# Kernel optimization log

Hardware: AMD Instinct MI355X
Metric: run time of the kernel (lower is better)

## Reference

```python
import jax, jax.numpy as jnp
import numpy as np

NEG_SLOPE = 0.2  # GAT LeakyReLU slope
EPS = 1e-16


def _pagat_conv(x, path_index, W, a, b, heads, out_ch, concat):
    """Path-augmented GAT conv: attention over (head, mid, tail) path triples,
    messages flow tail -> head, softmax-normalized per destination node."""
    N = x.shape[0]
    head, mid, tail = path_index[0], path_index[1], path_index[2]
    h = (x @ W).reshape(N, heads, out_ch)            # [N, H, C]
    # attention logits from all three path positions: [P, H]
    e = (jnp.einsum('phc,hc->ph', h[head], a[0])
         + jnp.einsum('phc,hc->ph', h[mid], a[1])
         + jnp.einsum('phc,hc->ph', h[tail], a[2]))
    e = jax.nn.leaky_relu(e, NEG_SLOPE)
    # segment softmax over paths grouped by destination (head) node
    m = jax.ops.segment_max(e, head, num_segments=N)  # [N, H]
    ex = jnp.exp(e - m[head])
    s = jax.ops.segment_sum(ex, head, num_segments=N)  # [N, H]
    alpha = ex / (s[head] + EPS)                       # [P, H]
    # aggregate tail features weighted by attention
    out = jax.ops.segment_sum(alpha[..., None] * h[tail], head, num_segments=N)  # [N, H, C]
    if concat:
        out = out.reshape(N, heads * out_ch)
    else:
        out = out.mean(axis=1)
    return out + b


def setup_inputs() -> dict:
    key = jax.random.key(0)
    ks = jax.random.split(key, 8)
    N, F_in, H, C, CLS, P = 100000, 500, 8, 16, 16, 1000000
    x = jax.random.normal(ks[0], (N, F_in), dtype=jnp.float32)
    path_index = jax.random.randint(ks[1], (3, P), 0, N, dtype=jnp.int32)
    W1 = jax.random.normal(ks[2], (F_in, H * C), dtype=jnp.float32) * 0.05
    a1 = jax.random.normal(ks[3], (3, H, C), dtype=jnp.float32) * 0.05
    b1 = jnp.zeros((H * C,), dtype=jnp.float32)
    W2 = jax.random.normal(ks[4], (H * C, CLS), dtype=jnp.float32) * 0.05
    a2 = jax.random.normal(ks[5], (3, 1, CLS), dtype=jnp.float32) * 0.05
    b2 = jnp.zeros((CLS,), dtype=jnp.float32)
    return {"x": x, "path_index": path_index, "W1": W1, "a1": a1, "b1": b1,
            "W2": W2, "a2": a2, "b2": b2}


def reference(x, path_index, W1, a1, b1, W2, a2, b2):
    # eval mode: dropout is identity
    h = _pagat_conv(x, path_index, W1, a1, b1, heads=8, out_ch=16, concat=True)
    h = jax.nn.elu(h)
    h = _pagat_conv(h, path_index, W2, a2, b2, heads=1, out_ch=16, concat=False)
    return jax.nn.log_softmax(h, axis=1)
```

## Files before the change

### kernel.cpp

```cpp
#include <hip/hip_runtime.h>
#include <hip/hip_bf16.h>

#define F_IN  500
#define HC    128
#define NHEAD 8
#define CDIM  16
#define NCLS  16
#define KPAD  512

static __device__ __forceinline__ float bf(const __hip_bfloat16 v) {
    return __bfloat162float(v);
}

static __device__ __forceinline__ unsigned int enc_f32(float f) {
    unsigned int u = __float_as_uint(f);
    return (u & 0x80000000u) ? ~u : (u | 0x80000000u);
}
static __device__ __forceinline__ float dec_f32(unsigned int u) {
    return __uint_as_float((u & 0x80000000u) ? (u & 0x7FFFFFFFu) : ~u);
}

typedef __bf16 bf16x8 __attribute__((ext_vector_type(8)));
typedef float f32x4 __attribute__((ext_vector_type(4)));

__global__ void zero_i32(int* __restrict__ p, int n) {
    int i = blockIdx.x * blockDim.x + threadIdx.x;
    if (i < n) p[i] = 0;
}

__global__ void transpose_w1(const float* __restrict__ W1,
                             __bf16* __restrict__ w1t_hi,
                             __bf16* __restrict__ w1t_lo)
{
    int id = blockIdx.x * 256 + threadIdx.x;
    int c = id >> 9, k = id & 511;
    float v = (k < F_IN) ? W1[k * HC + c] : 0.f;
    __bf16 h = (__bf16)v;
    w1t_hi[id] = h;
    w1t_lo[id] = (__bf16)(v - (float)h);
}

static __device__ __forceinline__ void split8(const float4 a, const float4 b,
                                              bf16x8& hi, bf16x8& lo) {
    float v[8] = {a.x, a.y, a.z, a.w, b.x, b.y, b.z, b.w};
#pragma unroll
    for (int j = 0; j < 8; j++) {
        __bf16 h = (__bf16)v[j];
        hi[j] = h;
        lo[j] = (__bf16)(v[j] - (float)h);
    }
}

__global__ __launch_bounds__(256) void gemm1_mfma(
    const float* __restrict__ x,
    const __bf16* __restrict__ w1t_hi, const __bf16* __restrict__ w1t_lo,
    __hip_bfloat16* __restrict__ h1, int N)
{
    const int wave = threadIdx.x >> 6, lane = threadIdx.x & 63;
    const int m = lane & 15, q = lane >> 4;
    const int row0 = blockIdx.x * 128 + wave * 32;

    long ra0 = row0 + m, ra1 = row0 + 16 + m;
    if (ra0 >= N) ra0 = 0;
    if (ra1 >= N) ra1 = 0;
    const float* pa0 = x + ra0 * F_IN + q * 8;
    const float* pa1 = x + ra1 * F_IN + q * 8;
    const __bf16* pbh = w1t_hi + (size_t)m * KPAD + q * 8;
    const __bf16* pbl = w1t_lo + (size_t)m * KPAD + q * 8;

    f32x4 acc[2][8];
#pragma unroll
    for (int i = 0; i < 2; i++)
#pragma unroll
        for (int t = 0; t < 8; t++) acc[i][t] = (f32x4){0.f, 0.f, 0.f, 0.f};

#pragma unroll
    for (int k0 = 0; k0 < 480; k0 += 32) {
        bf16x8 a0h, a0l, a1h, a1l;
        split8(*(const float4*)(pa0 + k0), *(const float4*)(pa0 + k0 + 4), a0h, a0l);
        split8(*(const float4*)(pa1 + k0), *(const float4*)(pa1 + k0 + 4), a1h, a1l);
#pragma unroll
        for (int t = 0; t < 8; t++) {
            bf16x8 bh = *(const bf16x8*)(pbh + t * 16 * KPAD + k0);
            bf16x8 bl = *(const bf16x8*)(pbl + t * 16 * KPAD + k0);
            acc[0][t] = __builtin_amdgcn_mfma_f32_16x16x32_bf16(a0h, bh, acc[0][t], 0, 0, 0);
            acc[0][t] = __builtin_amdgcn_mfma_f32_16x16x32_bf16(a0h, bl, acc[0][t], 0, 0, 0);
            acc[0][t] = __builtin_amdgcn_mfma_f32_16x16x32_bf16(a0l, bh, acc[0][t], 0, 0, 0);
            acc[1][t] = __builtin_amdgcn_mfma_f32_16x16x32_bf16(a1h, bh, acc[1][t], 0, 0, 0);
            acc[1][t] = __builtin_amdgcn_mfma_f32_16x16x32_bf16(a1h, bl, acc[1][t], 0, 0, 0);
            acc[1][t] = __builtin_amdgcn_mfma_f32_16x16x32_bf16(a1l, bh, acc[1][t], 0, 0, 0);
        }
    }
    {
        const float4 z4 = make_float4(0.f, 0.f, 0.f, 0.f);
        bf16x8 a0h, a0l, a1h, a1l;
        float4 u0 = (q < 3) ? *(const float4*)(pa0 + 480) : z4;
        float4 u1 = (q < 2) ? *(const float4*)(pa0 + 484) : z4;
        float4 w0 = (q < 3) ? *(const float4*)(pa1 + 480) : z4;
        float4 w1 = (q < 2) ? *(const float4*)(pa1 + 484) : z4;
        split8(u0, u1, a0h, a0l);
        split8(w0, w1, a1h, a1l);
#pragma unroll
        for (int t = 0; t < 8; t++) {
            bf16x8 bh = *(const bf16x8*)(pbh + t * 16 * KPAD + 480);
            bf16x8 bl = *(const bf16x8*)(pbl + t * 16 * KPAD + 480);
            acc[0][t] = __builtin_amdgcn_mfma_f32_16x16x32_bf16(a0h, bh, acc[0][t], 0, 0, 0);
            acc[0][t] = __builtin_amdgcn_mfma_f32_16x16x32_bf16(a0h, bl, acc[0][t], 0, 0, 0);
            acc[0][t] = __builtin_amdgcn_mfma_f32_16x16x32_bf16(a0l, bh, acc[0][t], 0, 0, 0);
            acc[1][t] = __builtin_amdgcn_mfma_f32_16x16x32_bf16(a1h, bh, acc[1][t], 0, 0, 0);
            acc[1][t] = __builtin_amdgcn_mfma_f32_16x16x32_bf16(a1h, bl, acc[1][t], 0, 0, 0);
            acc[1][t] = __builtin_amdgcn_mfma_f32_16x16x32_bf16(a1l, bh, acc[1][t], 0, 0, 0);
        }
    }
#pragma unroll
    for (int rt = 0; rt < 2; rt++) {
        int rbase = row0 + rt * 16 + q * 4;
#pragma unroll
        for (int t = 0; t < 8; t++) {
#pragma unroll
            for (int r = 0; r < 4; r++) {
                int row = rbase + r;
                if (row < N)
                    h1[(size_t)row * HC + t * 16 + m] = __float2bfloat16(acc[rt][t][r]);
            }
        }
    }
}

__global__ void dots1_kernel(const __hip_bfloat16* __restrict__ h1,
                             const float* __restrict__ a1,
                             float* __restrict__ d1, int N)
{
    int id = blockIdx.x * blockDim.x + threadIdx.x;
    if (id >= N * NHEAD) return;
    int n = id >> 3, h = id & 7;
    const __hip_bfloat16* hp = h1 + (size_t)n * HC + h * CDIM;
    float s0 = 0.f, s1 = 0.f, s2 = 0.f;
#pragma unroll
    for (int c = 0; c < CDIM; c++) {
        float v = bf(hp[c]);
        s0 += v * a1[(0 * NHEAD + h) * CDIM + c];
        s1 += v * a1[(1 * NHEAD + h) * CDIM + c];
        s2 += v * a1[(2 * NHEAD + h) * CDIM + c];
    }
    d1[id] = s0;
    d1[N * NHEAD + id] = s1;
    d1[2 * N * NHEAD + id] = s2;
}

__global__ void maxred_d1(const float* __restrict__ d1,
                          unsigned int* __restrict__ gmax, int N)
{
    __shared__ unsigned int sm[16];
    if (threadIdx.x < 16) sm[threadIdx.x] = 0;
    __syncthreads();
    int total = 2 * N * NHEAD;
    for (int i = blockIdx.x * blockDim.x + threadIdx.x; i < total;
         i += gridDim.x * blockDim.x) {
        float v = d1[(size_t)N * NHEAD + i];
        int slot = ((i >= N * NHEAD) ? 8 : 0) + (i & 7);
        atomicMax(&sm[slot], enc_f32(v));
    }
    __syncthreads();
    if (threadIdx.x < 16) atomicMax(&gmax[threadIdx.x], sm[threadIdx.x]);
}

__global__ void maxred_d2(const float* __restrict__ d2,
                          unsigned int* __restrict__ gmax2, int N)
{
    __shared__ unsigned int sm[2];
    if (threadIdx.x < 2) sm[threadIdx.x] = 0;
    __syncthreads();
    int total = 2 * N;
    for (int i = blockIdx.x * blockDim.x + threadIdx.x; i < total;
         i += gridDim.x * blockDim.x) {
        float v = d2[N + i];
        atomicMax(&sm[i >= N ? 1 : 0], enc_f32(v));
    }
    __syncthreads();
    if (threadIdx.x < 2) atomicMax(&gmax2[threadIdx.x], sm[threadIdx.x]);
}

__global__ void hist_kernel(const int* __restrict__ pidx, int* __restrict__ deg, int P) {
    int p = blockIdx.x * blockDim.x + threadIdx.x;
    if (p < P) atomicAdd(deg + pidx[p], 1);
}

__global__ void scan1_kernel(const int* __restrict__ deg, int* __restrict__ start,
                             int* __restrict__ bsum, int N) {
    __shared__ int sh[256];
    int i = blockIdx.x * 256 + threadIdx.x;
    int v = (i < N) ? deg[i] : 0;
    sh[threadIdx.x] = v;
    __syncthreads();
#pragma unroll
    for (int off = 1; off < 256; off <<= 1) {
        int x = (threadIdx.x >= off) ? sh[threadIdx.x - off] : 0;
        __syncthreads();
        sh[threadIdx.x] += x;
        __syncthreads();
    }
    if (i < N) start[i] = sh[threadIdx.x] - v;
    if (threadIdx.x == 255) bsum[blockIdx.x] = sh[255];
}

__global__ void scan2_kernel(int* __restrict__ bsum, int nb) {
    __shared__ int sh[512];
    int v = (threadIdx.x < nb) ? bsum[threadIdx.x] : 0;
    sh[threadIdx.x] = v;
    __syncthreads();
#pragma unroll
    for (int off = 1; off < 512; off <<= 1) {
        int x = (threadIdx.x >= off) ? sh[threadIdx.x - off] : 0;
        __syncthreads();
        sh[threadIdx.x] += x;
        __syncthreads();
    }
    if (threadIdx.x < nb) bsum[threadIdx.x] = sh[threadIdx.x] - v;
}

__global__ void scan3_kernel(int* __restrict__ start, const int* __restrict__ bsum, int N) {
    int i = blockIdx.x * 256 + threadIdx.x;
    if (i < N) start[i] += bsum[blockIdx.x];
}

__global__ void scatter_kernel(const int* __restrict__ pidx,
                               const int* __restrict__ start,
                               int* __restrict__ cursor,
                               int* __restrict__ csr, int P) {
    int p = blockIdx.x * blockDim.x + threadIdx.x;
    if (p >= P) return;
    int hd = pidx[p];
    int pos = atomicAdd(cursor + hd, 1);
    csr[start[hd] + pos] = p;
}

__global__ __launch_bounds__(256) void attn1_csr_kernel(
    const int* __restrict__ csr, const int* __restrict__ start,
    const int* __restrict__ deg, const int* __restrict__ pidx,
    const float* __restrict__ d1, const __hip_bfloat16* __restrict__ h1,
    const float* __restrict__ b1, const unsigned int* __restrict__ gmax,
    float* __restrict__ elu_out, int N, int P)
{
    int node = blockIdx.x * 4 + (threadIdx.x >> 6);
    if (node >= N) return;
    int lane = threadIdx.x & 63;
    int h = lane >> 3;
    int s0 = start[node], dg = deg[node];
    const float* d1m = d1 + (size_t)N * NHEAD;
    const float* d1t = d1 + (size_t)2 * N * NHEAD;
    const float dh = d1[node * NHEAD + h];
    float zub = dh + dec_f32(gmax[h]) + dec_f32(gmax[8 + h]);
    const float mxub = zub > 0.f ? zub : 0.2f * zub;

    float acc0 = 0.f, acc1 = 0.f, den = 0.f;
    for (int k0 = 0; k0 < dg; k0 += 8) {
        int kk = k0 + (lane & 7);
        bool valid = kk < dg;
        int p = csr[s0 + (valid ? kk : dg - 1)];
        int mid = pidx[P + p], tl = pidx[2 * P + p];
        float z = dh + d1m[mid * NHEAD + h] + d1t[tl * NHEAD + h];
        float e = z > 0.f ? z : 0.2f * z;
        float ex = valid ? __expf(e - mxub) : 0.f;
        den += ex;
        int kmax = dg - k0; if (kmax > 8) kmax = 8;
        for (int dk = 0; dk < kmax; dk++) {
            int tl_b = __shfl(tl, dk, 8);
            float ex_b = __shfl(ex, dk, 8);
            __hip_bfloat162 v = *(const __hip_bfloat162*)(h1 + (size_t)tl_b * HC + 2 * lane);
            acc0 += ex_b * bf(v.x);
            acc1 += ex_b * bf(v.y);
        }
    }
#pragma unroll
    for (int w = 1; w < 8; w <<= 1) den += __shfl_xor(den, w, 8);

    float inv = 1.f / (den + 1e-16f);
    int j0 = 2 * lane;
    float v0 = acc0 * inv + b1[j0];
    float v1 = acc1 * inv + b1[j0 + 1];
    v0 = v0 > 0.f ? v0 : __expf(v0) - 1.f;
    v1 = v1 > 0.f ? v1 : __expf(v1) - 1.f;
    *(float2*)(elu_out + (size_t)node * HC + j0) = make_float2(v0, v1);
}

__global__ __launch_bounds__(256) void layer2_kernel(
    const float* __restrict__ elu, const float* __restrict__ W2,
    const float* __restrict__ a2,
    float* __restrict__ h2, float* __restrict__ d2, int N)
{
    __shared__ float rows[16][HC + 1];
    __shared__ float h2s[16][NCLS + 1];
    const int n0 = blockIdx.x * 16;
    const int tid = threadIdx.x;
    for (int idx = tid; idx < 16 * HC; idx += 256) {
        int r = idx >> 7, c = idx & 127;
        rows[r][c] = (n0 + r < N) ? elu[(size_t)(n0 + r) * HC + c] : 0.f;
    }
    __syncthreads();
    int ln = tid >> 4, c = tid & 15;
    float acc = 0.f;
#pragma unroll 8
    for (int j = 0; j < HC; j++) acc += rows[ln][j] * W2[j * NCLS + c];
    h2s[ln][c] = acc;
    if (n0 + ln < N) h2[(size_t)(n0 + ln) * NCLS + c] = acc;
    __syncthreads();
    if (tid < 48) {
        int l = tid / 3, j = tid - l * 3;
        if (n0 + l < N) {
            float s = 0.f;
#pragma unroll
            for (int cc = 0; cc < NCLS; cc++) s += h2s[l][cc] * a2[j * NCLS + cc];
            d2[j * N + n0 + l] = s;
        }
    }
}

__global__ __launch_bounds__(256) void attn2_csr_kernel(
    const int* __restrict__ csr, const int* __restrict__ start,
    const int* __restrict__ deg, const int* __restrict__ pidx,
    const float* __restrict__ d2, const float* __restrict__ h2,
    const float* __restrict__ b2, const unsigned int* __restrict__ gmax2,
    float* __restrict__ out, int N, int P)
{
    int node = blockIdx.x * 16 + (threadIdx.x >> 4);
    if (node >= N) return;
    int c = threadIdx.x & 15;
    int s0 = start[node], dg = deg[node];
    const float dh = d2[node];
    const float* d2m = d2 + N;
    const float* d2t = d2 + 2 * N;
    float zub = dh + dec_f32(gmax2[0]) + dec_f32(gmax2[1]);
    const float mxub = zub > 0.f ? zub : 0.2f * zub;

    float acc = 0.f, den = 0.f;
    for (int k0 = 0; k0 < dg; k0 += 16) {
        int kk = k0 + c;
        bool valid = kk < dg;
        int p = csr[s0 + (valid ? kk : dg - 1)];
        int mid = pidx[P + p], tl = pidx[2 * P + p];
        float z = dh + d2m[mid] + d2t[tl];
        float e = z > 0.f ? z : 0.2f * z;
        float ex = valid ? __expf(e - mxub) : 0.f;
        den += ex;
        int kmax = dg - k0; if (kmax > 16) kmax = 16;
        for (int dk = 0; dk < kmax; dk++) {
            int tl_b = __shfl(tl, dk, 16);
            float ex_b = __shfl(ex, dk, 16);
            acc += ex_b * h2[(size_t)tl_b * NCLS + c];
        }
    }
#pragma unroll
    for (int w = 1; w < 16; w <<= 1) den += __shfl_xor(den, w, 16);

    float o = acc / (den + 1e-16f) + b2[c];
    float m2 = o;
#pragma unroll
    for (int w = 1; w < 16; w <<= 1) m2 = fmaxf(m2, __shfl_xor(m2, w, 16));
    float ex = __expf(o - m2), sm = ex;
#pragma unroll
    for (int w = 1; w < 16; w <<= 1) sm += __shfl_xor(sm, w, 16);
    float r = o - m2 - __logf(sm);
    out[(size_t)node * NCLS + c] = r;
}

extern "C" void kernel_launch(void* const* d_in, const int* in_sizes, int n_in,
                              void* d_out, int out_size, void* d_ws, size_t ws_size,
                              hipStream_t stream)
{
    const float* x  = (const float*)d_in[0];
    const int*   pi = (const int*)d_in[1];
    const float* W1 = (const float*)d_in[2];
    const float* a1 = (const float*)d_in[3];
    const float* b1 = (const float*)d_in[4];
    const float* W2 = (const float*)d_in[5];
    const float* a2 = (const float*)d_in[6];
    const float* b2 = (const float*)d_in[7];

    const int N = in_sizes[0] / F_IN;
    const int P = in_sizes[1] / 3;

    float* ws = (float*)d_ws;
    size_t off_h1     = 0;
    size_t off_d1     = (size_t)64 * N;
    size_t off_elu    = (size_t)88 * N;
    size_t off_h2     = (size_t)216 * N;
    size_t off_d2     = (size_t)232 * N;
    size_t off_deg    = (size_t)235 * N;
    size_t off_start  = (size_t)236 * N;
    size_t off_cursor = (size_t)237 * N;
    size_t off_gmax   = (size_t)238 * N;
    size_t off_bsum   = (size_t)238 * N + 32;
    size_t off_csr    = (size_t)238 * N + 32 + 1024;
    size_t off_w1th   = off_csr + P;
    size_t off_w1tl   = off_w1th + 32768;

    __hip_bfloat16* h1 = (__hip_bfloat16*)(ws + off_h1);
    float* d1   = ws + off_d1;
    float* elu  = ws + off_elu;
    float* h2   = ws + off_h2;
    float* d2   = ws + off_d2;
    int* deg    = (int*)(ws + off_deg);
    int* start  = (int*)(ws + off_start);
    int* cursor = (int*)(ws + off_cursor);
    unsigned int* gmax  = (unsigned int*)(ws + off_gmax);
    unsigned int* gmax2 = (unsigned int*)(ws + off_gmax) + 16;
    int* bsum   = (int*)(ws + off_bsum);
    int* csr    = (int*)(ws + off_csr);
    __bf16* w1t_hi = (__bf16*)(ws + off_w1th);
    __bf16* w1t_lo = (__bf16*)(ws + off_w1tl);

    const int BLK = 256;
    const int nb = (N + 255) / 256;

    transpose_w1<<<(HC * KPAD) / 256, 256, 0, stream>>>(W1, w1t_hi, w1t_lo);
    zero_i32<<<(3 * N + 32 + BLK - 1) / BLK, BLK, 0, stream>>>(deg, 3 * N + 32);
    gemm1_mfma<<<(N + 127) / 128, 256, 0, stream>>>(x, w1t_hi, w1t_lo, h1, N);
    dots1_kernel<<<(N * NHEAD + BLK - 1) / BLK, BLK, 0, stream>>>(h1, a1, d1, N);
    maxred_d1<<<1024, 256, 0, stream>>>(d1, gmax, N);
    hist_kernel<<<(P + BLK - 1) / BLK, BLK, 0, stream>>>(pi, deg, P);
    scan1_kernel<<<nb, 256, 0, stream>>>(deg, start, bsum, N);
    scan2_kernel<<<1, 512, 0, stream>>>(bsum, nb);
    scan3_kernel<<<nb, 256, 0, stream>>>(start, bsum, N);
    scatter_kernel<<<(P + BLK - 1) / BLK, BLK, 0, stream>>>(pi, start, cursor, csr, P);
    attn1_csr_kernel<<<(N + 3) / 4, 256, 0, stream>>>(csr, start, deg, pi, d1, h1, b1, gmax, elu, N, P);
    layer2_kernel<<<(N + 15) / 16, 256, 0, stream>>>(elu, W2, a2, h2, d2, N);
    maxred_d2<<<256, 256, 0, stream>>>(d2, gmax2, N);
    attn2_csr_kernel<<<(N + 15) / 16, 256, 0, stream>>>(csr, start, deg, pi, d2, h2, b2, gmax2,
                                                        (float*)d_out, N, P);
}
```

Baseline: 735.3 us.

## Stage GEMM1 tiles through LDS with double-buffered async global-to-LDS loads

New measurement: 701.3 us. -4.6%, faster.

```diff
diff --git a/kernel.cpp b/kernel.cpp
--- a/kernel.cpp
+++ b/kernel.cpp
@@ -23,6 +23,12 @@
 typedef __bf16 bf16x8 __attribute__((ext_vector_type(8)));
 typedef float f32x4 __attribute__((ext_vector_type(4)));
 
+static __device__ __forceinline__ void gload16(const void* g, void* l) {
+    __builtin_amdgcn_global_load_lds(
+        (const __attribute__((address_space(1))) void*)g,
+        (__attribute__((address_space(3))) void*)l, 16, 0, 0);
+}
+
 __global__ void zero_i32(int* __restrict__ p, int n) {
     int i = blockIdx.x * blockDim.x + threadIdx.x;
     if (i < n) p[i] = 0;
@@ -51,77 +57,104 @@
     }
 }
 
-__global__ __launch_bounds__(256) void gemm1_mfma(
+__global__ __launch_bounds__(256, 3) void gemm1_v2(
     const float* __restrict__ x,
-    const __bf16* __restrict__ w1t_hi, const __bf16* __restrict__ w1t_lo,
+    const __bf16* __restrict__ w1hi, const __bf16* __restrict__ w1lo,
+    const float* __restrict__ zpad,
     __hip_bfloat16* __restrict__ h1, int N)
 {
-    const int wave = threadIdx.x >> 6, lane = threadIdx.x & 63;
+    __shared__ float As[2][64 * 32];
+    __shared__ __bf16 BsH[2][128 * 32];
+    __shared__ __bf16 BsL[2][128 * 32];
+
+    const int tid = threadIdx.x;
+    const int lane = tid & 63, wave = tid >> 6;
     const int m = lane & 15, q = lane >> 4;
-    const int row0 = blockIdx.x * 128 + wave * 32;
-
-    long ra0 = row0 + m, ra1 = row0 + 16 + m;
-    if (ra0 >= N) ra0 = 0;
-    if (ra1 >= N) ra1 = 0;
-    const float* pa0 = x + ra0 * F_IN + q * 8;
-    const float* pa1 = x + ra1 * F_IN + q * 8;
-    const __bf16* pbh = w1t_hi + (size_t)m * KPAD + q * 8;
-    const __bf16* pbl = w1t_lo + (size_t)m * KPAD + q * 8;
-
-    f32x4 acc[2][8];
-#pragma unroll
-    for (int i = 0; i < 2; i++)
-#pragma unroll
-        for (int t = 0; t < 8; t++) acc[i][t] = (f32x4){0.f, 0.f, 0.f, 0.f};
-
-#pragma unroll
-    for (int k0 = 0; k0 < 480; k0 += 32) {
-        bf16x8 a0h, a0l, a1h, a1l;
-        split8(*(const float4*)(pa0 + k0), *(const float4*)(pa0 + k0 + 4), a0h, a0l);
-        split8(*(const float4*)(pa1 + k0), *(const float4*)(pa1 + k0 + 4), a1h, a1l);
-#pragma unroll
-        for (int t = 0; t < 8; t++) {
-            bf16x8 bh = *(const bf16x8*)(pbh + t * 16 * KPAD + k0);
-            bf16x8 bl = *(const bf16x8*)(pbl + t * 16 * KPAD + k0);
-            acc[0][t] = __builtin_amdgcn_mfma_f32_16x16x32_bf16(a0h, bh, acc[0][t], 0, 0, 0);
-            acc[0][t] = __builtin_amdgcn_mfma_f32_16x16x32_bf16(a0h, bl, acc[0][t], 0, 0, 0);
-            acc[0][t] = __builtin_amdgcn_mfma_f32_16x16x32_bf16(a0l, bh, acc[0][t], 0, 0, 0);
-            acc[1][t] = __builtin_amdgcn_mfma_f32_16x16x32_bf16(a1h, bh, acc[1][t], 0, 0, 0);
-            acc[1][t] = __builtin_amdgcn_mfma_f32_16x16x32_bf16(a1h, bl, acc[1][t], 0, 0, 0);
-            acc[1][t] = __builtin_amdgcn_mfma_f32_16x16x32_bf16(a1l, bh, acc[1][t], 0, 0, 0);
-        }
-    }
-    {
-        const float4 z4 = make_float4(0.f, 0.f, 0.f, 0.f);
-        bf16x8 a0h, a0l, a1h, a1l;
-        float4 u0 = (q < 3) ? *(const float4*)(pa0 + 480) : z4;
-        float4 u1 = (q < 2) ? *(const float4*)(pa0 + 484) : z4;
-        float4 w0 = (q < 3) ? *(const float4*)(pa1 + 480) : z4;
-        float4 w1 = (q < 2) ? *(const float4*)(pa1 + 484) : z4;
-        split8(u0, u1, a0h, a0l);
-        split8(w0, w1, a1h, a1l);
-#pragma unroll
-        for (int t = 0; t < 8; t++) {
-            bf16x8 bh = *(const bf16x8*)(pbh + t * 16 * KPAD + 480);
-            bf16x8 bl = *(const bf16x8*)(pbl + t * 16 * KPAD + 480);
-            acc[0][t] = __builtin_amdgcn_mfma_f32_16x16x32_bf16(a0h, bh, acc[0][t], 0, 0, 0);
-            acc[0][t] = __builtin_amdgcn_mfma_f32_16x16x32_bf16(a0h, bl, acc[0][t], 0, 0, 0);
-            acc[0][t] = __builtin_amdgcn_mfma_f32_16x16x32_bf16(a0l, bh, acc[0][t], 0, 0, 0);
-            acc[1][t] = __builtin_amdgcn_mfma_f32_16x16x32_bf16(a1h, bh, acc[1][t], 0, 0, 0);
-            acc[1][t] = __builtin_amdgcn_mfma_f32_16x16x32_bf16(a1h, bl, acc[1][t], 0, 0, 0);
-            acc[1][t] = __builtin_amdgcn_mfma_f32_16x16x32_bf16(a1l, bh, acc[1][t], 0, 0, 0);
-        }
-    }
-#pragma unroll
-    for (int rt = 0; rt < 2; rt++) {
-        int rbase = row0 + rt * 16 + q * 4;
-#pragma unroll
-        for (int t = 0; t < 8; t++) {
-#pragma unroll
-            for (int r = 0; r < 4; r++) {
+    const int wr = wave >> 1, wc = wave & 1;
+    const int n0 = blockIdx.x * 64;
+    const int woff = (tid >> 6) << 10;
+
+    auto stage = [&](int buf, int t) {
+        const int k0 = t * 32;
+#pragma unroll
+        for (int j = 0; j < 2; ++j) {
+            int idx = j * 256 + tid;
+            {
+                int r = idx >> 3, ps = idx & 7;
+                int ls = ps ^ (r & 7);
+                int kk = k0 + ls * 4;
+                int grow = n0 + r;
+                const float* src = (kk < F_IN)
+                    ? (x + (size_t)(grow < N ? grow : 0) * F_IN + kk)
+                    : zpad;
+                gload16(src, (char*)&As[buf][0] + j * 4096 + woff);
+            }
+            {
+                int c = idx >> 2, ps2 = idx & 3;
+                int ls2 = ps2 ^ (c & 3);
+                const __bf16* sh = w1hi + c * KPAD + k0 + ls2 * 8;
+                const __bf16* sl = w1lo + c * KPAD + k0 + ls2 * 8;
+                gload16(sh, (char*)&BsH[buf][0] + j * 4096 + woff);
+                gload16(sl, (char*)&BsL[buf][0] + j * 4096 + woff);
+            }
+        }
+    };
+
+    f32x4 acc[2][4];
+#pragma unroll
+    for (int rt = 0; rt < 2; ++rt)
+#pragma unroll
+        for (int ct = 0; ct < 4; ++ct) acc[rt][ct] = (f32x4){0.f, 0.f, 0.f, 0.f};
+
+    stage(0, 0);
+    __syncthreads();
+    int cur = 0;
+
+#pragma unroll 2
+    for (int t = 0; t < 16; ++t) {
+        if (t < 15) stage(cur ^ 1, t + 1);
+
+        bf16x8 ah[2], al[2];
+#pragma unroll
+        for (int rt = 0; rt < 2; ++rt) {
+            int r = wr * 32 + rt * 16 + m;
+            int x7 = r & 7;
+            const float4* rowp = (const float4*)&As[cur][r * 32];
+            float4 f0 = rowp[(2 * q) ^ x7];
+            float4 f1 = rowp[(2 * q + 1) ^ x7];
+            split8(f0, f1, ah[rt], al[rt]);
+        }
+        bf16x8 bh[4], bl[4];
+#pragma unroll
+        for (int ct = 0; ct < 4; ++ct) {
+            int c = wc * 64 + ct * 16 + m;
+            int s = q ^ (c & 3);
+            bh[ct] = *(const bf16x8*)&BsH[cur][c * 32 + s * 8];
+            bl[ct] = *(const bf16x8*)&BsL[cur][c * 32 + s * 8];
+        }
+#pragma unroll
+        for (int rt = 0; rt < 2; ++rt)
+#pragma unroll
+            for (int ct = 0; ct < 4; ++ct) {
+                acc[rt][ct] = __builtin_amdgcn_mfma_f32_16x16x32_bf16(ah[rt], bh[ct], acc[rt][ct], 0, 0, 0);
+                acc[rt][ct] = __builtin_amdgcn_mfma_f32_16x16x32_bf16(ah[rt], bl[ct], acc[rt][ct], 0, 0, 0);
+                acc[rt][ct] = __builtin_amdgcn_mfma_f32_16x16x32_bf16(al[rt], bh[ct], acc[rt][ct], 0, 0, 0);
+            }
+        __syncthreads();
+        cur ^= 1;
+    }
+
+#pragma unroll
+    for (int rt = 0; rt < 2; ++rt) {
+        int rbase = n0 + wr * 32 + rt * 16 + q * 4;
+#pragma unroll
+        for (int ct = 0; ct < 4; ++ct) {
+            int col = wc * 64 + ct * 16 + m;
+#pragma unroll
+            for (int r = 0; r < 4; ++r) {
                 int row = rbase + r;
                 if (row < N)
-                    h1[(size_t)row * HC + t * 16 + m] = __float2bfloat16(acc[rt][t][r]);
+                    h1[(size_t)row * HC + col] = __float2bfloat16(acc[rt][ct][r]);
             }
         }
     }
@@ -390,8 +423,9 @@
     size_t off_start  = (size_t)236 * N;
     size_t off_cursor = (size_t)237 * N;
     size_t off_gmax   = (size_t)238 * N;
-    size_t off_bsum   = (size_t)238 * N + 32;
-    size_t off_csr    = (size_t)238 * N + 32 + 1024;
+    size_t off_zpad   = (size_t)238 * N + 32;
+    size_t off_bsum   = (size_t)238 * N + 96;
+    size_t off_csr    = (size_t)238 * N + 96 + 1024;
     size_t off_w1th   = off_csr + P;
     size_t off_w1tl   = off_w1th + 32768;
 
@@ -405,6 +439,7 @@
     int* cursor = (int*)(ws + off_cursor);
     unsigned int* gmax  = (unsigned int*)(ws + off_gmax);
     unsigned int* gmax2 = (unsigned int*)(ws + off_gmax) + 16;
+    float* zpad = ws + off_zpad;
     int* bsum   = (int*)(ws + off_bsum);
     int* csr    = (int*)(ws + off_csr);
     __bf16* w1t_hi = (__bf16*)(ws + off_w1th);
@@ -414,8 +449,8 @@
     const int nb = (N + 255) / 256;
 
     transpose_w1<<<(HC * KPAD) / 256, 256, 0, stream>>>(W1, w1t_hi, w1t_lo);
-    zero_i32<<<(3 * N + 32 + BLK - 1) / BLK, BLK, 0, stream>>>(deg, 3 * N + 32);
-    gemm1_mfma<<<(N + 127) / 128, 256, 0, stream>>>(x, w1t_hi, w1t_lo, h1, N);
+    zero_i32<<<(3 * N + 96 + BLK - 1) / BLK, BLK, 0, stream>>>(deg, 3 * N + 96);
+    gemm1_v2<<<(N + 63) / 64, 256, 0, stream>>>(x, w1t_hi, w1t_lo, zpad, h1, N);
     dots1_kernel<<<(N * NHEAD + BLK - 1) / BLK, BLK, 0, stream>>>(h1, a1, d1, N);
     maxred_d1<<<1024, 256, 0, stream>>>(d1, gmax, N);
     hist_kernel<<<(P + BLK - 1) / BLK, BLK, 0, stream>>>(pi, deg, P);
```
